# Performance work log

Hardware: AMD Instinct MI355X
Metric: run time of the kernel (lower is better)

## Reference

```python
import jax, jax.numpy as jnp
import numpy as np

N_NODES = 100000
N_EDGES = 600000
D = 128
N_TYPES = 3


def setup_inputs() -> dict:
    key = jax.random.key(0)
    ks = jax.random.split(key, 10)
    x = jax.random.normal(ks[0], (N_NODES, D), dtype=jnp.float32)
    edge_index = jax.random.randint(ks[1], (2, N_EDGES), 0, N_NODES, dtype=jnp.int64)
    edge_type_ids = jax.random.randint(ks[2], (N_EDGES,), 0, N_TYPES, dtype=jnp.int32)
    edge_weights = jax.random.uniform(ks[3], (N_EDGES,), dtype=jnp.float32)
    # Xavier-uniform linear weights (in==out==D), zero biases, uniform attention
    limit = float(np.sqrt(6.0 / (D + D)))
    W_edge = jax.random.uniform(ks[4], (N_TYPES, D, D), minval=-limit, maxval=limit, dtype=jnp.float32)
    b_edge = jnp.zeros((N_TYPES, D), dtype=jnp.float32)
    W_self = jax.random.uniform(ks[5], (D, D), minval=-limit, maxval=limit, dtype=jnp.float32)
    b_self = jnp.zeros((D,), dtype=jnp.float32)
    attention = jnp.ones((N_TYPES + 1,), dtype=jnp.float32) / (N_TYPES + 1)
    return {"x": x, "edge_index": edge_index, "edge_type_ids": edge_type_ids,
            "edge_weights": edge_weights, "W_edge": W_edge, "b_edge": b_edge,
            "W_self": W_self, "b_self": b_self, "attention": attention}


def reference(x, edge_index, edge_type_ids, edge_weights, W_edge, b_edge, W_self, b_self, attention):
    n_nodes = x.shape[0]
    n_types = W_edge.shape[0]
    src, dst = edge_index[0], edge_index[1]
    xs = x[src]  # (E, D) gather once, shared by all edge types
    outs = []
    for t in range(n_types):  # small fixed set of structurally distinct linears
        # mask zeros out edges of other types; equivalent to torch's boolean slicing
        m = jnp.where(edge_type_ids == t, edge_weights, jnp.zeros((), x.dtype))
        y = (xs @ W_edge[t] + b_edge[t]) * m[:, None]  # (E, D)
        outs.append(jax.ops.segment_sum(y, dst, num_segments=n_nodes))  # scatter-add
    outs.append(x @ W_self + b_self)
    stacked = jnp.stack(outs, axis=-1)  # (N, D, n_types+1)
    attn = jax.nn.softmax(attention)
    out = jnp.sum(stacked * attn, axis=-1)
    return jax.nn.gelu(out, approximate=False)  # torch F.gelu default is erf-based
```

## Files before the change

### kernel.cpp

```cpp
#include <hip/hip_runtime.h>
#include <hip/hip_bf16.h>
#include <math.h>

#define D 128
#define NT 3
#define KTOT (D * (NT + 1))

typedef __attribute__((ext_vector_type(8))) __bf16 bf16x8;
typedef __attribute__((ext_vector_type(4))) float f32x4;

__device__ inline unsigned short f2bf(float f) {
    unsigned int u = __float_as_uint(f);
    unsigned int r = (u + 0x7FFFu + ((u >> 16) & 1u)) >> 16;
    return (unsigned short)r;
}

__global__ void zero_kernel(float* __restrict__ p, long long n4) {
    long long i = (long long)blockIdx.x * blockDim.x + threadIdx.x;
    long long stride = (long long)gridDim.x * blockDim.x;
    float4 z = make_float4(0.f, 0.f, 0.f, 0.f);
    for (; i < n4; i += stride) ((float4*)p)[i] = z;
}

__global__ void zeroi_kernel(int* __restrict__ p, int n) {
    int i = blockIdx.x * blockDim.x + threadIdx.x;
    int st = gridDim.x * blockDim.x;
    for (; i < n; i += st) p[i] = 0;
}

__global__ void prep_kernel(const float* __restrict__ W_edge, const float* __restrict__ b_edge,
                            const float* __restrict__ W_self, const float* __restrict__ b_self,
                            const float* __restrict__ attention,
                            float* __restrict__ wcat, float* __restrict__ biasb,
                            unsigned short* __restrict__ bfrag) {
    float a0 = attention[0], a1 = attention[1], a2 = attention[2], a3 = attention[3];
    float m = fmaxf(fmaxf(a0, a1), fmaxf(a2, a3));
    float e0 = expf(a0 - m), e1 = expf(a1 - m), e2 = expf(a2 - m), e3 = expf(a3 - m);
    float inv = 1.f / (e0 + e1 + e2 + e3);
    float at[4] = {e0 * inv, e1 * inv, e2 * inv, e3 * inv};

    int idx0 = blockIdx.x * blockDim.x + threadIdx.x;
    int stride = gridDim.x * blockDim.x;
    for (int i = idx0; i < KTOT * D; i += stride) {
        int k = i >> 7, j = i & (D - 1);
        float v;
        if (k < D) {
            v = at[NT] * W_self[k * D + j];
        } else {
            int t = (k - D) >> 7;
            int kk = (k - D) & (D - 1);
            v = at[t] * W_edge[(t * D + kk) * D + j];
        }
        wcat[i] = v;
    }
    for (int i = idx0; i < KTOT; i += stride) {
        if (i < NT * D) {
            int t = i >> 7, j = i & (D - 1);
            biasb[i] = at[t] * b_edge[t * D + j];
        } else {
            biasb[i] = at[NT] * b_self[i - NT * D];
        }
    }
    for (int i = idx0; i < 16 * 8 * 64; i += stride) {
        int l = i & 63;
        int cf = (i >> 6) & 7;
        int step = i >> 9;
        int col = cf * 16 + (l & 15);
        int kb = step * 32 + ((l >> 4) * 8);
#pragma unroll
        for (int j = 0; j < 8; ++j) {
            int k = kb + j;
            float v;
            if (k < D) {
                v = at[NT] * W_self[k * D + col];
            } else {
                int t = (k - D) >> 7;
                int kk = (k - D) & (D - 1);
                v = at[t] * W_edge[(t * D + kk) * D + col];
            }
            bfrag[(size_t)i * 8 + j] = f2bf(v);
        }
    }
}

__global__ __launch_bounds__(256) void xcvt_kernel(
    const float* __restrict__ x, unsigned short* __restrict__ ab, int nN) {
    int i = blockIdx.x * blockDim.x + threadIdx.x;
    int total = nN * (D / 4);
    int stride = gridDim.x * blockDim.x;
    for (; i < total; i += stride) {
        int n = i >> 5;
        int c4 = (i & 31) * 4;
        float4 v = *(const float4*)(x + (size_t)n * D + c4);
        ushort4 o;
        o.x = f2bf(v.x); o.y = f2bf(v.y); o.z = f2bf(v.z); o.w = f2bf(v.w);
        *(ushort4*)(ab + (size_t)n * 512 + c4) = o;
    }
}

__global__ __launch_bounds__(256) void fill_kernel(
    const int* __restrict__ ei, const int* __restrict__ et, const float* __restrict__ ew,
    int* __restrict__ deg, int2* __restrict__ csr, int* __restrict__ ovfcnt,
    int* __restrict__ ovflist, int nE, int cap) {
    int e = blockIdx.x * blockDim.x + threadIdx.x;
    if (e >= nE) return;
    int dst = ei[nE + e];
    int pos = atomicAdd(deg + dst, 1);
    if (pos < cap) {
        int src = ei[e];
        int t = et[e];
        csr[(size_t)dst * cap + pos] = make_int2(src | (t << 20), __float_as_int(ew[e]));
    } else {
        int o = atomicAdd(ovfcnt, 1);
        ovflist[o] = e;
    }
}

__global__ __launch_bounds__(256) void gatherb_kernel(
    const int2* __restrict__ csr, const int* __restrict__ deg,
    unsigned short* __restrict__ ab, float* __restrict__ s, int nN, int cap) {
    int wid = (blockIdx.x * blockDim.x + threadIdx.x) >> 6;
    int lane = threadIdx.x & 63;
    int gl = lane & 15;
    int base = lane & 48;
    int node = wid * 4 + (lane >> 4);
    int nclamp = (node < nN) ? node : (nN - 1);
    int dg = deg[nclamp];
    if (dg > cap) dg = cap;
    if (node >= nN) dg = 0;
    const int2* c = csr + (size_t)nclamp * cap;
    int2 mA = (gl < dg) ? c[gl] : make_int2(0, 0);
    int2 mB = (gl + 16 < dg) ? c[gl + 16] : make_int2(0, 0);

    float ac0[8], ac1[8], ac2[8];
#pragma unroll
    for (int j = 0; j < 8; ++j) { ac0[j] = 0.f; ac1[j] = 0.f; ac2[j] = 0.f; }
    float sw0 = 0.f, sw1 = 0.f, sw2 = 0.f;

    for (int i = 0; i < dg; i += 2) {
        int slA = base + (i & 15);
        int exA = __shfl((i < 16) ? mA.x : mB.x, slA);
        int ewA = __shfl((i < 16) ? mA.y : mB.y, slA);
        int srcA = exA & 0xFFFFF;
        if (srcA >= nN) srcA = 0;
        float wA = __int_as_float(ewA);
        int tA = (exA >> 20) & 3;
        bool actB = (i + 1 < dg);
        int slB = base + ((i + 1) & 15);
        int exB = __shfl((i + 1 < 16) ? mA.x : mB.x, slB);
        int ewB = __shfl((i + 1 < 16) ? mA.y : mB.y, slB);
        int srcB = exB & 0xFFFFF;
        if (!actB || srcB >= nN) srcB = 0;
        float wB = actB ? __int_as_float(ewB) : 0.f;
        int tB = (exB >> 20) & 3;

        uint4 xa = *(const uint4*)(ab + (size_t)srcA * 512 + gl * 8);
        uint4 xb = *(const uint4*)(ab + (size_t)srcB * 512 + gl * 8);

        float wA0 = (tA == 0) ? wA : 0.f;
        float wA1 = (tA == 1) ? wA : 0.f;
        float wA2 = (tA == 2) ? wA : 0.f;
        float wB0 = (tB == 0) ? wB : 0.f;
        float wB1 = (tB == 1) ? wB : 0.f;
        float wB2 = (tB == 2) ? wB : 0.f;
        sw0 += wA0 + wB0; sw1 += wA1 + wB1; sw2 += wA2 + wB2;

        float f0, f1;
#define ACCUM(u, j0, j1, w0_, w1_, w2_)                                   \
        f0 = __uint_as_float((u) << 16);                                  \
        f1 = __uint_as_float((u) & 0xFFFF0000u);                          \
        ac0[j0] = fmaf(w0_, f0, ac0[j0]); ac0[j1] = fmaf(w0_, f1, ac0[j1]); \
        ac1[j0] = fmaf(w1_, f0, ac1[j0]); ac1[j1] = fmaf(w1_, f1, ac1[j1]); \
        ac2[j0] = fmaf(w2_, f0, ac2[j0]); ac2[j1] = fmaf(w2_, f1, ac2[j1]);

        ACCUM(xa.x, 0, 1, wA0, wA1, wA2)
        ACCUM(xa.y, 2, 3, wA0, wA1, wA2)
        ACCUM(xa.z, 4, 5, wA0, wA1, wA2)
        ACCUM(xa.w, 6, 7, wA0, wA1, wA2)
        ACCUM(xb.x, 0, 1, wB0, wB1, wB2)
        ACCUM(xb.y, 2, 3, wB0, wB1, wB2)
        ACCUM(xb.z, 4, 5, wB0, wB1, wB2)
        ACCUM(xb.w, 6, 7, wB0, wB1, wB2)
#undef ACCUM
    }

    if (node < nN) {
        unsigned short* ap = ab + (size_t)node * 512 + D;
        uint4 o;
#define PACK(arr)                                                           \
        o.x = (unsigned int)f2bf(arr[0]) | ((unsigned int)f2bf(arr[1]) << 16); \
        o.y = (unsigned int)f2bf(arr[2]) | ((unsigned int)f2bf(arr[3]) << 16); \
        o.z = (unsigned int)f2bf(arr[4]) | ((unsigned int)f2bf(arr[5]) << 16); \
        o.w = (unsigned int)f2bf(arr[6]) | ((unsigned int)f2bf(arr[7]) << 16);
        PACK(ac0) *(uint4*)(ap + 0 * D + gl * 8) = o;
        PACK(ac1) *(uint4*)(ap + 1 * D + gl * 8) = o;
        PACK(ac2) *(uint4*)(ap + 2 * D + gl * 8) = o;
#undef PACK
        if (gl < 3) {
            float sv = (gl == 0) ? sw0 : ((gl == 1) ? sw1 : sw2);
            s[(size_t)node * NT + gl] = sv;
        }
    }
}

__global__ __launch_bounds__(64) void ovf_fix_kernel(
    const int* __restrict__ ei, const int* __restrict__ et, const float* __restrict__ ew,
    const int* __restrict__ ovfcnt, const int* __restrict__ ovflist,
    unsigned short* __restrict__ ab, float* __restrict__ s, int nE) {
    int cnt = *ovfcnt;
    int lane = threadIdx.x;
    for (int i = 0; i < cnt; ++i) {
        int e = ovflist[i];
        int src = ei[e], dst = ei[nE + e], t = et[e];
        float w = ew[e];
        unsigned int xu = *(const unsigned int*)(ab + (size_t)src * 512 + lane * 2);
        float x0 = __uint_as_float(xu << 16);
        float x1 = __uint_as_float(xu & 0xFFFF0000u);
        unsigned short* p = ab + (size_t)dst * 512 + D + t * D + lane * 2;
        unsigned int au = *(unsigned int*)p;
        float v0 = __uint_as_float(au << 16) + w * x0;
        float v1 = __uint_as_float(au & 0xFFFF0000u) + w * x1;
        *(unsigned int*)p = (unsigned int)f2bf(v0) | ((unsigned int)f2bf(v1) << 16);
        if (lane == 0) s[(size_t)dst * NT + t] += w;
        __builtin_amdgcn_s_barrier();
    }
}

__global__ __launch_bounds__(256, 4) void mfma_gemm_kernel(
    const unsigned short* __restrict__ ab, const unsigned short* __restrict__ bfrag,
    const float* __restrict__ s, const float* __restrict__ biasb,
    float* __restrict__ out, int nN) {
    __shared__ unsigned char lds[32768];
    int t = threadIdx.x;
    int w = t >> 6;
    int lane = t & 63;
    int wr = w >> 1, wc = w & 1;
    int ll = lane & 15;
    int ck = lane >> 4;
    long row0 = (long)blockIdx.x * 128;

    int srow = t >> 2;
    int clin = t & 3;
    int ssw = (srow & 3) ^ ((srow >> 2) & 3);
    int cg = clin ^ ssw;
    long nodeA0 = row0 + srow;       if (nodeA0 >= nN) nodeA0 = nN - 1;
    long nodeA1 = row0 + 64 + srow;  if (nodeA1 >= nN) nodeA1 = nN - 1;
    const unsigned short* gA0 = ab + nodeA0 * 512 + cg * 8;
    const unsigned short* gA1 = ab + nodeA1 * 512 + cg * 8;
    const unsigned short* gB0 = bfrag + ((size_t)w * 64 + lane) * 8;
    const unsigned short* gB1 = bfrag + ((size_t)(4 + w) * 64 + lane) * 8;

#define STAGE(buf, st_) do {                                                            \
        unsigned char* la0 = lds + (buf) * 8192 + w * 1024;                             \
        unsigned char* la1 = lds + (buf) * 8192 + 4096 + w * 1024;                      \
        unsigned char* lb0 = lds + 16384 + (buf) * 8192 + w * 1024;                     \
        unsigned char* lb1 = lds + 16384 + (buf) * 8192 + 4096 + w * 1024;              \
        __builtin_amdgcn_global_load_lds((const __attribute__((address_space(1))) void*)(gA0 + (st_) * 32),            \
                                         (__attribute__((address_space(3))) void*)la0, 16, 0, 0);                      \
        __builtin_amdgcn_global_load_lds((const __attribute__((address_space(1))) void*)(gA1 + (st_) * 32),            \
                                         (__attribute__((address_space(3))) void*)la1, 16, 0, 0);                      \
        __builtin_amdgcn_global_load_lds((const __attribute__((address_space(1))) void*)(gB0 + (size_t)(st_) * 4096),  \
                                         (__attribute__((address_space(3))) void*)lb0, 16, 0, 0);                      \
        __builtin_amdgcn_global_load_lds((const __attribute__((address_space(1))) void*)(gB1 + (size_t)(st_) * 4096),  \
                                         (__attribute__((address_space(3))) void*)lb1, 16, 0, 0);                      \
    } while (0)

    int rsw = (ll & 3) ^ ((ll >> 2) & 3);
    int aoffBase = (wr * 64 + ll) * 64 + ((ck ^ rsw) * 16);
    int boffBase = 16384 + (wc * 4) * 1024 + lane * 16;

    f32x4 acc[4][4];
#pragma unroll
    for (int i = 0; i < 4; ++i)
#pragma unroll
        for (int j = 0; j < 4; ++j) acc[i][j] = (f32x4){0.f, 0.f, 0.f, 0.f};

    STAGE(0, 0);
    __syncthreads();

#pragma unroll 2
    for (int st = 0; st < 16; ++st) {
        int cur = st & 1;
        if (st < 15) STAGE(cur ^ 1, st + 1);
        const unsigned char* A = lds + cur * 8192;
        const unsigned char* B = lds + cur * 8192;
        bf16x8 aF[4], bF[4];
#pragma unroll
        for (int fr = 0; fr < 4; ++fr)
            aF[fr] = *(const bf16x8*)(A + aoffBase + fr * 1024);
#pragma unroll
        for (int fc = 0; fc < 4; ++fc)
            bF[fc] = *(const bf16x8*)(B + boffBase + fc * 1024);
#pragma unroll
        for (int fr = 0; fr < 4; ++fr)
#pragma unroll
            for (int fc = 0; fc < 4; ++fc)
                acc[fr][fc] = __builtin_amdgcn_mfma_f32_16x16x32_bf16(aF[fr], bF[fc], acc[fr][fc], 0, 0, 0);
        __syncthreads();
    }
#undef STAGE

    long wrow0 = row0 + wr * 64;
    int colb = wc * 64 + ll;
    float bb0[4], bb1[4], bb2[4], bs4[4];
#pragma unroll
    for (int fc = 0; fc < 4; ++fc) {
        int c = colb + fc * 16;
        bb0[fc] = biasb[c]; bb1[fc] = biasb[D + c];
        bb2[fc] = biasb[2 * D + c]; bs4[fc] = biasb[3 * D + c];
    }
    const float kInvSqrt2 = 0.70710678118654752440f;
#pragma unroll
    for (int fr = 0; fr < 4; ++fr) {
#pragma unroll
        for (int reg = 0; reg < 4; ++reg) {
            long row = wrow0 + fr * 16 + (lane >> 4) * 4 + reg;
            if (row >= nN) continue;
            float s0 = s[row * NT + 0];
            float s1 = s[row * NT + 1];
            float s2 = s[row * NT + 2];
#pragma unroll
            for (int fc = 0; fc < 4; ++fc) {
                float v = acc[fr][fc][reg] + bs4[fc] + s0 * bb0[fc] + s1 * bb1[fc] + s2 * bb2[fc];
                v = 0.5f * v * (1.f + erff(v * kInvSqrt2));
                out[row * D + colb + fc * 16] = v;
            }
        }
    }
}

__global__ __launch_bounds__(256) void scatterA_kernel(
    const float* __restrict__ x, const int* __restrict__ ei,
    const int* __restrict__ et, const float* __restrict__ ew,
    float* __restrict__ agg, float* __restrict__ s, int nE) {
    int gtid = blockIdx.x * blockDim.x + threadIdx.x;
    int wave = gtid >> 6;
    int lane = threadIdx.x & 63;
    int nw = (gridDim.x * blockDim.x) >> 6;
    for (int e = wave; e < nE; e += nw) {
        int src = ei[e];
        int dst = ei[nE + e];
        int t = et[e];
        float w = ew[e];
        float2 xv = *(const float2*)(x + (size_t)src * D + lane * 2);
        float* p = agg + (size_t)dst * (NT * D) + t * D + lane * 2;
        unsafeAtomicAdd(p, w * xv.x);
        unsafeAtomicAdd(p + 1, w * xv.y);
        if (lane == 0) unsafeAtomicAdd(s + (size_t)dst * NT + t, w);
    }
}

#define BM 64
#define BK 32
__global__ __launch_bounds__(256) void gemm_gelu_kernel(
    const float* __restrict__ x, const float* __restrict__ agg,
    const float* __restrict__ s, const float* __restrict__ wcat,
    const float* __restrict__ biasb, float* __restrict__ out, int nNodes) {
    __shared__ float As[BK][BM + 1];
    __shared__ float Bs[BK][D];

    int tx = threadIdx.x;
    int row0 = blockIdx.x * BM;
    int cg = tx & 31;
    int rg = tx >> 5;
    int lr = tx >> 3;
    int lc = (tx & 7) * 4;

    float acc[8][4];
#pragma unroll
    for (int i = 0; i < 8; ++i)
#pragma unroll
        for (int j = 0; j < 4; ++j) acc[i][j] = 0.f;

    for (int k0 = 0; k0 < KTOT; k0 += BK) {
        const float* srcBase;
        int strideA, koff;
        if (k0 < D) { srcBase = x; strideA = D; koff = k0; }
        else        { srcBase = agg; strideA = NT * D; koff = k0 - D; }
#pragma unroll
        for (int h = 0; h < 2; ++h) {
            int r = lr + h * 32;
            int node = row0 + r;
            if (node >= nNodes) node = nNodes - 1;
            float4 v = *(const float4*)(srcBase + (size_t)node * strideA + koff + lc);
            As[lc + 0][r] = v.x; As[lc + 1][r] = v.y;
            As[lc + 2][r] = v.z; As[lc + 3][r] = v.w;
        }
        {
            int br = tx >> 5;
            int bc = (tx & 31) * 4;
#pragma unroll
            for (int h = 0; h < 4; ++h) {
                int r = br + h * 8;
                *(float4*)(&Bs[r][bc]) = *(const float4*)(wcat + (size_t)(k0 + r) * D + bc);
            }
        }
        __syncthreads();
#pragma unroll
        for (int kk = 0; kk < BK; ++kk) {
            float4 b = *(const float4*)(&Bs[kk][cg * 4]);
            float a[8];
            *(float4*)(a)     = *(const float4*)(&As[kk][rg * 8]);
            *(float4*)(a + 4) = *(const float4*)(&As[kk][rg * 8 + 4]);
#pragma unroll
            for (int i = 0; i < 8; ++i) {
                acc[i][0] = fmaf(a[i], b.x, acc[i][0]);
                acc[i][1] = fmaf(a[i], b.y, acc[i][1]);
                acc[i][2] = fmaf(a[i], b.z, acc[i][2]);
                acc[i][3] = fmaf(a[i], b.w, acc[i][3]);
            }
        }
        __syncthreads();
    }

    int jc = cg * 4;
    float4 bb0 = *(const float4*)(biasb + 0 * D + jc);
    float4 bb1 = *(const float4*)(biasb + 1 * D + jc);
    float4 bb2 = *(const float4*)(biasb + 2 * D + jc);
    float4 bsv = *(const float4*)(biasb + NT * D + jc);
#pragma unroll
    for (int i = 0; i < 8; ++i) {
        int node = row0 + rg * 8 + i;
        if (node >= nNodes) break;
        float s0 = s[(size_t)node * NT + 0];
        float s1 = s[(size_t)node * NT + 1];
        float s2 = s[(size_t)node * NT + 2];
        float4 r;
        r.x = acc[i][0] + bsv.x + s0 * bb0.x + s1 * bb1.x + s2 * bb2.x;
        r.y = acc[i][1] + bsv.y + s0 * bb0.y + s1 * bb1.y + s2 * bb2.y;
        r.z = acc[i][2] + bsv.z + s0 * bb0.z + s1 * bb1.z + s2 * bb2.z;
        r.w = acc[i][3] + bsv.w + s0 * bb0.w + s1 * bb1.w + s2 * bb2.w;
        const float kInvSqrt2 = 0.70710678118654752440f;
        r.x = 0.5f * r.x * (1.f + erff(r.x * kInvSqrt2));
        r.y = 0.5f * r.y * (1.f + erff(r.y * kInvSqrt2));
        r.z = 0.5f * r.z * (1.f + erff(r.z * kInvSqrt2));
        r.w = 0.5f * r.w * (1.f + erff(r.w * kInvSqrt2));
        *(float4*)(out + (size_t)node * D + jc) = r;
    }
}

__global__ __launch_bounds__(256) void selfmv_kernel(
    const float* __restrict__ x, const float* __restrict__ Ws,
    const float* __restrict__ bs, const float* __restrict__ attn,
    float* __restrict__ out, int nN) {
    float a0 = attn[0], a1 = attn[1], a2 = attn[2], a3 = attn[3];
    float m = fmaxf(fmaxf(a0, a1), fmaxf(a2, a3));
    float e3 = expf(a3 - m);
    float inv = 1.f / (expf(a0 - m) + expf(a1 - m) + expf(a2 - m) + e3);
    float at3 = e3 * inv;
    int wave = (blockIdx.x * blockDim.x + threadIdx.x) >> 6;
    int lane = threadIdx.x & 63;
    int nw = (gridDim.x * blockDim.x) >> 6;
    for (int n = wave; n < nN; n += nw) {
        float2 xr = *(const float2*)(x + (size_t)n * D + lane * 2);
        float acc0 = 0.f, acc1 = 0.f;
#pragma unroll
        for (int k = 0; k < D; ++k) {
            float xv = __shfl((k & 1) ? xr.y : xr.x, k >> 1);
            float2 wv = *(const float2*)(Ws + (size_t)k * D + lane * 2);
            acc0 = fmaf(xv, wv.x, acc0);
            acc1 = fmaf(xv, wv.y, acc1);
        }
        float2 r;
        r.x = at3 * (acc0 + bs[lane * 2]);
        r.y = at3 * (acc1 + bs[lane * 2 + 1]);
        *(float2*)(out + (size_t)n * D + lane * 2) = r;
    }
}

__global__ __launch_bounds__(256) void edgemv_kernel(
    const float* __restrict__ x, const int* __restrict__ ei,
    const int* __restrict__ et, const float* __restrict__ ew,
    const float* __restrict__ We, const float* __restrict__ be,
    const float* __restrict__ attn, float* __restrict__ out, int nE) {
    float a0 = attn[0], a1 = attn[1], a2 = attn[2], a3 = attn[3];
    float m = fmaxf(fmaxf(a0, a1), fmaxf(a2, a3));
    float e0 = expf(a0 - m), e1 = expf(a1 - m), e2 = expf(a2 - m), e3 = expf(a3 - m);
    float inv = 1.f / (e0 + e1 + e2 + e3);
    float at[NT] = {e0 * inv, e1 * inv, e2 * inv};
    int wave = (blockIdx.x * blockDim.x + threadIdx.x) >> 6;
    int lane = threadIdx.x & 63;
    int nw = (gridDim.x * blockDim.x) >> 6;
    for (int e = wave; e < nE; e += nw) {
        int src = ei[e];
        int dst = ei[nE + e];
        int t = et[e];
        float sc = ew[e] * at[t];
        const float* W = We + (size_t)t * D * D;
        float2 xr = *(const float2*)(x + (size_t)src * D + lane * 2);
        float acc0 = 0.f, acc1 = 0.f;
#pragma unroll
        for (int k = 0; k < D; ++k) {
            float xv = __shfl((k & 1) ? xr.y : xr.x, k >> 1);
            float2 wv = *(const float2*)(W + (size_t)k * D + lane * 2);
            acc0 = fmaf(xv, wv.x, acc0);
            acc1 = fmaf(xv, wv.y, acc1);
        }
        float* p = out + (size_t)dst * D + lane * 2;
        unsafeAtomicAdd(p,     sc * (acc0 + be[(size_t)t * D + lane * 2]));
        unsafeAtomicAdd(p + 1, sc * (acc1 + be[(size_t)t * D + lane * 2 + 1]));
    }
}

__global__ void gelu_kernel(float* __restrict__ p, long long n4) {
    long long i = (long long)blockIdx.x * blockDim.x + threadIdx.x;
    long long stride = (long long)gridDim.x * blockDim.x;
    const float kInvSqrt2 = 0.70710678118654752440f;
    for (; i < n4; i += stride) {
        float4 r = ((float4*)p)[i];
        r.x = 0.5f * r.x * (1.f + erff(r.x * kInvSqrt2));
        r.y = 0.5f * r.y * (1.f + erff(r.y * kInvSqrt2));
        r.z = 0.5f * r.z * (1.f + erff(r.z * kInvSqrt2));
        r.w = 0.5f * r.w * (1.f + erff(r.w * kInvSqrt2));
        ((float4*)p)[i] = r;
    }
}

extern "C" void kernel_launch(void* const* d_in, const int* in_sizes, int n_in,
                              void* d_out, int out_size, void* d_ws, size_t ws_size,
                              hipStream_t stream) {
    const float* x = (const float*)d_in[0];
    const int* ei = (const int*)d_in[1];
    const int* et = (const int*)d_in[2];
    const float* ew = (const float*)d_in[3];
    const float* W_edge = (const float*)d_in[4];
    const float* b_edge = (const float*)d_in[5];
    const float* W_self = (const float*)d_in[6];
    const float* b_self = (const float*)d_in[7];
    const float* attention = (const float*)d_in[8];
    float* out = (float*)d_out;

    const int nN = in_sizes[0] / D;
    const int nE = in_sizes[2];

    int cap = 0;
    const int capCand[3] = {32, 24, 16};
    for (int ci = 0; ci < 3; ++ci) {
        int c = capCand[ci];
        size_t need = (size_t)nN * 1024
                    + (size_t)nN * 12
                    + (size_t)KTOT * D * 4
                    + (size_t)KTOT * 4
                    + 131072
                    + 4 * ((size_t)nN + 2 + (size_t)nE)
                    + 8ull * nN * c;
        if (ws_size >= need) { cap = c; break; }
    }

    if (cap > 0) {
        unsigned short* ab = (unsigned short*)d_ws;
        float* sW = (float*)(ab + (size_t)nN * 512);
        float* wcat = sW + (size_t)nN * NT;
        float* biasb = wcat + (size_t)KTOT * D;
        unsigned short* bfrag = (unsigned short*)(biasb + KTOT);
        int* deg = (int*)(bfrag + 65536);
        int* ovfc = deg + nN;
        int* ovfl = ovfc + 2;
        int2* csr = (int2*)(ovfl + nE);

        hipLaunchKernelGGL(zeroi_kernel, dim3(128), dim3(256), 0, stream, deg, nN + 2);
        hipLaunchKernelGGL(prep_kernel, dim3(64), dim3(256), 0, stream,
                           W_edge, b_edge, W_self, b_self, attention, wcat, biasb, bfrag);
        hipLaunchKernelGGL(xcvt_kernel, dim3(2048), dim3(256), 0, stream, x, ab, nN);
        hipLaunchKernelGGL(fill_kernel, dim3((nE + 255) / 256), dim3(256), 0, stream,
                           ei, et, ew, deg, csr, ovfc, ovfl, nE, cap);
        hipLaunchKernelGGL(gatherb_kernel, dim3((nN + 15) / 16), dim3(256), 0, stream,
                           csr, deg, ab, sW, nN, cap);
        hipLaunchKernelGGL(ovf_fix_kernel, dim3(1), dim3(64), 0, stream,
                           ei, et, ew, ovfc, ovfl, ab, sW, nE);
        hipLaunchKernelGGL(mfma_gemm_kernel, dim3((nN + 127) / 128), dim3(256), 0, stream,
                           ab, bfrag, sW, biasb, out, nN);
        return;
    }

    const size_t baseFloats = (size_t)nN * NT * D + (size_t)nN * NT + (size_t)KTOT * D + KTOT;
    if (ws_size >= baseFloats * 4) {
        float* agg = (float*)d_ws;
        float* sW = agg + (size_t)nN * NT * D;
        float* wcat = sW + (size_t)nN * NT;
        float* biasb = wcat + (size_t)KTOT * D;
        long long zeroFloats = (long long)nN * (NT * D + NT);
        hipLaunchKernelGGL(zero_kernel, dim3(2048), dim3(256), 0, stream, agg, (zeroFloats + 3) / 4);
        hipLaunchKernelGGL(prep_kernel, dim3(64), dim3(256), 0, stream,
                           W_edge, b_edge, W_self, b_self, attention, wcat, biasb, (unsigned short*)wcat );
        hipLaunchKernelGGL(scatterA_kernel, dim3(2048), dim3(256), 0, stream,
                           x, ei, et, ew, agg, sW, nE);
        hipLaunchKernelGGL(gemm_gelu_kernel, dim3((nN + BM - 1) / BM), dim3(256), 0, stream,
                           x, agg, sW, wcat, biasb, out, nN);
    } else {
        hipLaunchKernelGGL(selfmv_kernel, dim3(2048), dim3(256), 0, stream,
                           x, W_self, b_self, attention, out, nN);
        hipLaunchKernelGGL(edgemv_kernel, dim3(2048), dim3(256), 0, stream,
                           x, ei, et, ew, W_edge, b_edge, attention, out, nE);
        hipLaunchKernelGGL(gelu_kernel, dim3(2048), dim3(256), 0, stream,
                           out, (long long)nN * D / 4);
    }
}
```

Baseline: 130.6 us.

## Fuse zeroing into prep, merge xcvt with fill, halve GEMM row tile

Degree zeroing moves into prep_kernel and the x-to-bf16 conversion is merged with the CSR fill kernel, which removes two kernel launches and lets the two independent workloads run concurrently. The MFMA GEMM tile goes from 128 to 64 rows per block, with less LDS and fewer accumulators, so it launches more blocks with higher occupancy. In exchange, the smaller tile reloads the B fragments more often per output row.

```diff
diff --git a/kernel.cpp b/kernel.cpp
--- a/kernel.cpp
+++ b/kernel.cpp
@@ -22,17 +22,12 @@
     for (; i < n4; i += stride) ((float4*)p)[i] = z;
 }
 
-__global__ void zeroi_kernel(int* __restrict__ p, int n) {
-    int i = blockIdx.x * blockDim.x + threadIdx.x;
-    int st = gridDim.x * blockDim.x;
-    for (; i < n; i += st) p[i] = 0;
-}
-
 __global__ void prep_kernel(const float* __restrict__ W_edge, const float* __restrict__ b_edge,
                             const float* __restrict__ W_self, const float* __restrict__ b_self,
                             const float* __restrict__ attention,
                             float* __restrict__ wcat, float* __restrict__ biasb,
-                            unsigned short* __restrict__ bfrag) {
+                            unsigned short* __restrict__ bfrag,
+                            int* __restrict__ deg, int degN) {
     float a0 = attention[0], a1 = attention[1], a2 = attention[2], a3 = attention[3];
     float m = fmaxf(fmaxf(a0, a1), fmaxf(a2, a3));
     float e0 = expf(a0 - m), e1 = expf(a1 - m), e2 = expf(a2 - m), e3 = expf(a3 - m);
@@ -41,6 +36,9 @@
 
     int idx0 = blockIdx.x * blockDim.x + threadIdx.x;
     int stride = gridDim.x * blockDim.x;
+    if (deg) {
+        for (int i = idx0; i < degN; i += stride) deg[i] = 0;
+    }
     for (int i = idx0; i < KTOT * D; i += stride) {
         int k = i >> 7, j = i & (D - 1);
         float v;
@@ -83,36 +81,37 @@
     }
 }
 
-__global__ __launch_bounds__(256) void xcvt_kernel(
-    const float* __restrict__ x, unsigned short* __restrict__ ab, int nN) {
-    int i = blockIdx.x * blockDim.x + threadIdx.x;
-    int total = nN * (D / 4);
-    int stride = gridDim.x * blockDim.x;
-    for (; i < total; i += stride) {
-        int n = i >> 5;
-        int c4 = (i & 31) * 4;
-        float4 v = *(const float4*)(x + (size_t)n * D + c4);
-        ushort4 o;
-        o.x = f2bf(v.x); o.y = f2bf(v.y); o.z = f2bf(v.z); o.w = f2bf(v.w);
-        *(ushort4*)(ab + (size_t)n * 512 + c4) = o;
-    }
-}
-
-__global__ __launch_bounds__(256) void fill_kernel(
+__global__ __launch_bounds__(256) void xcvt_fill_kernel(
+    const float* __restrict__ x, unsigned short* __restrict__ ab, int nN,
     const int* __restrict__ ei, const int* __restrict__ et, const float* __restrict__ ew,
     int* __restrict__ deg, int2* __restrict__ csr, int* __restrict__ ovfcnt,
-    int* __restrict__ ovflist, int nE, int cap) {
-    int e = blockIdx.x * blockDim.x + threadIdx.x;
-    if (e >= nE) return;
-    int dst = ei[nE + e];
-    int pos = atomicAdd(deg + dst, 1);
-    if (pos < cap) {
-        int src = ei[e];
-        int t = et[e];
-        csr[(size_t)dst * cap + pos] = make_int2(src | (t << 20), __float_as_int(ew[e]));
+    int* __restrict__ ovflist, int nE, int cap, int XB) {
+    int b = blockIdx.x;
+    if (b < XB) {
+        int i = b * 256 + threadIdx.x;
+        int total = nN * (D / 4);
+        int stride = XB * 256;
+        for (; i < total; i += stride) {
+            int n = i >> 5;
+            int c4 = (i & 31) * 4;
+            float4 v = *(const float4*)(x + (size_t)n * D + c4);
+            ushort4 o;
+            o.x = f2bf(v.x); o.y = f2bf(v.y); o.z = f2bf(v.z); o.w = f2bf(v.w);
+            *(ushort4*)(ab + (size_t)n * 512 + c4) = o;
+        }
     } else {
-        int o = atomicAdd(ovfcnt, 1);
-        ovflist[o] = e;
+        int e = (b - XB) * 256 + threadIdx.x;
+        if (e >= nE) return;
+        int dst = ei[nE + e];
+        int pos = atomicAdd(deg + dst, 1);
+        if (pos < cap) {
+            int src = ei[e];
+            int t = et[e];
+            csr[(size_t)dst * cap + pos] = make_int2(src | (t << 20), __float_as_int(ew[e]));
+        } else {
+            int o = atomicAdd(ovfcnt, 1);
+            ovflist[o] = e;
+        }
     }
 }
 
@@ -230,35 +229,30 @@
     const unsigned short* __restrict__ ab, const unsigned short* __restrict__ bfrag,
     const float* __restrict__ s, const float* __restrict__ biasb,
     float* __restrict__ out, int nN) {
-    __shared__ unsigned char lds[32768];
+    __shared__ unsigned char lds[24576];
     int t = threadIdx.x;
     int w = t >> 6;
     int lane = t & 63;
     int wr = w >> 1, wc = w & 1;
     int ll = lane & 15;
     int ck = lane >> 4;
-    long row0 = (long)blockIdx.x * 128;
+    long row0 = (long)blockIdx.x * 64;
 
     int srow = t >> 2;
     int clin = t & 3;
     int ssw = (srow & 3) ^ ((srow >> 2) & 3);
     int cg = clin ^ ssw;
-    long nodeA0 = row0 + srow;       if (nodeA0 >= nN) nodeA0 = nN - 1;
-    long nodeA1 = row0 + 64 + srow;  if (nodeA1 >= nN) nodeA1 = nN - 1;
-    const unsigned short* gA0 = ab + nodeA0 * 512 + cg * 8;
-    const unsigned short* gA1 = ab + nodeA1 * 512 + cg * 8;
+    long nodeA = row0 + srow; if (nodeA >= nN) nodeA = nN - 1;
+    const unsigned short* gA = ab + nodeA * 512 + cg * 8;
     const unsigned short* gB0 = bfrag + ((size_t)w * 64 + lane) * 8;
     const unsigned short* gB1 = bfrag + ((size_t)(4 + w) * 64 + lane) * 8;
 
 #define STAGE(buf, st_) do {                                                            \
-        unsigned char* la0 = lds + (buf) * 8192 + w * 1024;                             \
-        unsigned char* la1 = lds + (buf) * 8192 + 4096 + w * 1024;                      \
-        unsigned char* lb0 = lds + 16384 + (buf) * 8192 + w * 1024;                     \
-        unsigned char* lb1 = lds + 16384 + (buf) * 8192 + 4096 + w * 1024;              \
-        __builtin_amdgcn_global_load_lds((const __attribute__((address_space(1))) void*)(gA0 + (st_) * 32),            \
-                                         (__attribute__((address_space(3))) void*)la0, 16, 0, 0);                      \
-        __builtin_amdgcn_global_load_lds((const __attribute__((address_space(1))) void*)(gA1 + (st_) * 32),            \
-                                         (__attribute__((address_space(3))) void*)la1, 16, 0, 0);                      \
+        unsigned char* la  = lds + (buf) * 4096 + w * 1024;                             \
+        unsigned char* lb0 = lds + 8192 + (buf) * 8192 + w * 1024;                      \
+        unsigned char* lb1 = lds + 8192 + (buf) * 8192 + 4096 + w * 1024;               \
+        __builtin_amdgcn_global_load_lds((const __attribute__((address_space(1))) void*)(gA + (st_) * 32),             \
+                                         (__attribute__((address_space(3))) void*)la, 16, 0, 0);                       \
         __builtin_amdgcn_global_load_lds((const __attribute__((address_space(1))) void*)(gB0 + (size_t)(st_) * 4096),  \
                                          (__attribute__((address_space(3))) void*)lb0, 16, 0, 0);                      \
         __builtin_amdgcn_global_load_lds((const __attribute__((address_space(1))) void*)(gB1 + (size_t)(st_) * 4096),  \
@@ -266,12 +260,12 @@
     } while (0)
 
     int rsw = (ll & 3) ^ ((ll >> 2) & 3);
-    int aoffBase = (wr * 64 + ll) * 64 + ((ck ^ rsw) * 16);
-    int boffBase = 16384 + (wc * 4) * 1024 + lane * 16;
-
-    f32x4 acc[4][4];
-#pragma unroll
-    for (int i = 0; i < 4; ++i)
+    int aoffBase = (wr * 32 + ll) * 64 + ((ck ^ rsw) * 16);
+    int boffBase = 8192 + wc * 4096 + lane * 16;
+
+    f32x4 acc[2][4];
+#pragma unroll
+    for (int i = 0; i < 2; ++i)
 #pragma unroll
         for (int j = 0; j < 4; ++j) acc[i][j] = (f32x4){0.f, 0.f, 0.f, 0.f};
 
@@ -282,17 +276,17 @@
     for (int st = 0; st < 16; ++st) {
         int cur = st & 1;
         if (st < 15) STAGE(cur ^ 1, st + 1);
-        const unsigned char* A = lds + cur * 8192;
+        const unsigned char* A = lds + cur * 4096;
         const unsigned char* B = lds + cur * 8192;
-        bf16x8 aF[4], bF[4];
-#pragma unroll
-        for (int fr = 0; fr < 4; ++fr)
+        bf16x8 aF[2], bF[4];
+#pragma unroll
+        for (int fr = 0; fr < 2; ++fr)
             aF[fr] = *(const bf16x8*)(A + aoffBase + fr * 1024);
 #pragma unroll
         for (int fc = 0; fc < 4; ++fc)
             bF[fc] = *(const bf16x8*)(B + boffBase + fc * 1024);
 #pragma unroll
-        for (int fr = 0; fr < 4; ++fr)
+        for (int fr = 0; fr < 2; ++fr)
 #pragma unroll
             for (int fc = 0; fc < 4; ++fc)
                 acc[fr][fc] = __builtin_amdgcn_mfma_f32_16x16x32_bf16(aF[fr], bF[fc], acc[fr][fc], 0, 0, 0);
@@ -300,7 +294,7 @@
     }
 #undef STAGE
 
-    long wrow0 = row0 + wr * 64;
+    long wrow0 = row0 + wr * 32;
     int colb = wc * 64 + ll;
     float bb0[4], bb1[4], bb2[4], bs4[4];
 #pragma unroll
@@ -311,7 +305,7 @@
     }
     const float kInvSqrt2 = 0.70710678118654752440f;
 #pragma unroll
-    for (int fr = 0; fr < 4; ++fr) {
+    for (int fr = 0; fr < 2; ++fr) {
 #pragma unroll
         for (int reg = 0; reg < 4; ++reg) {
             long row = wrow0 + fr * 16 + (lane >> 4) * 4 + reg;
@@ -558,17 +552,18 @@
         int* ovfl = ovfc + 2;
         int2* csr = (int2*)(ovfl + nE);
 
-        hipLaunchKernelGGL(zeroi_kernel, dim3(128), dim3(256), 0, stream, deg, nN + 2);
         hipLaunchKernelGGL(prep_kernel, dim3(64), dim3(256), 0, stream,
-                           W_edge, b_edge, W_self, b_self, attention, wcat, biasb, bfrag);
-        hipLaunchKernelGGL(xcvt_kernel, dim3(2048), dim3(256), 0, stream, x, ab, nN);
-        hipLaunchKernelGGL(fill_kernel, dim3((nE + 255) / 256), dim3(256), 0, stream,
-                           ei, et, ew, deg, csr, ovfc, ovfl, nE, cap);
+                           W_edge, b_edge, W_self, b_self, attention, wcat, biasb, bfrag,
+                           deg, nN + 2);
+        const int XB = 512;
+        const int FB = (nE + 255) / 256;
+        hipLaunchKernelGGL(xcvt_fill_kernel, dim3(XB + FB), dim3(256), 0, stream,
+                           x, ab, nN, ei, et, ew, deg, csr, ovfc, ovfl, nE, cap, XB);
         hipLaunchKernelGGL(gatherb_kernel, dim3((nN + 15) / 16), dim3(256), 0, stream,
                            csr, deg, ab, sW, nN, cap);
         hipLaunchKernelGGL(ovf_fix_kernel, dim3(1), dim3(64), 0, stream,
                            ei, et, ew, ovfc, ovfl, ab, sW, nE);
-        hipLaunchKernelGGL(mfma_gemm_kernel, dim3((nN + 127) / 128), dim3(256), 0, stream,
+        hipLaunchKernelGGL(mfma_gemm_kernel, dim3((nN + 63) / 64), dim3(256), 0, stream,
                            ab, bfrag, sW, biasb, out, nN);
         return;
     }
@@ -582,7 +577,9 @@
         long long zeroFloats = (long long)nN * (NT * D + NT);
         hipLaunchKernelGGL(zero_kernel, dim3(2048), dim3(256), 0, stream, agg, (zeroFloats + 3) / 4);
         hipLaunchKernelGGL(prep_kernel, dim3(64), dim3(256), 0, stream,
-                           W_edge, b_edge, W_self, b_self, attention, wcat, biasb, (unsigned short*)wcat );
+                           W_edge, b_edge, W_self, b_self, attention, wcat, biasb,
+                           (unsigned short*)wcat ,
+                           (int*)nullptr, 0);
         hipLaunchKernelGGL(scatterA_kernel, dim3(2048), dim3(256), 0, stream,
                            x, ei, et, ew, agg, sW, nE);
         hipLaunchKernelGGL(gemm_gelu_kernel, dim3((nN + BM - 1) / BM), dim3(256), 0, stream,
```

New measurement: 124.7 us. 1.05x faster.
